# Performance work log

Hardware: AMD Instinct MI355X
Metric: run time of the kernel (lower is better)

The kernel has to match this reference:

```python
import jax, jax.numpy as jnp
import numpy as np

BN_EPS = 1e-5


def setup_inputs() -> dict:
    key = jax.random.key(0)
    ks = jax.random.split(key, 10)
    B, L, V, D = 4096, 200, 100000, 256
    tokens = jax.random.randint(ks[0], (B, L), 0, V, dtype=jnp.int32)
    lengths = jnp.maximum(jax.random.randint(ks[1], (B,), 0, L + 1, dtype=jnp.int32), 1)
    t = (jax.random.uniform(ks[2], (B,)) > 0.5).astype(jnp.float32)
    emb_table = jax.random.normal(ks[3], (V, D), dtype=jnp.float32)
    W1 = jax.random.normal(ks[4], (D, D), dtype=jnp.float32) * (1.0 / np.sqrt(D))
    b1 = jnp.zeros((D,), dtype=jnp.float32)
    gamma = jnp.ones((D,), dtype=jnp.float32)
    beta = jnp.zeros((D,), dtype=jnp.float32)
    w2 = jax.random.normal(ks[5], (D,), dtype=jnp.float32) * (1.0 / np.sqrt(D))
    b2 = jnp.zeros((), dtype=jnp.float32)
    return {"tokens": tokens, "lengths": lengths, "t": t, "emb_table": emb_table,
            "W1": W1, "b1": b1, "gamma": gamma, "beta": beta, "w2": w2, "b2": b2}


def reference(tokens, lengths, t, emb_table, W1, b1, gamma, beta, w2, b2):
    B, L = tokens.shape
    # ragged gather + mean pool (EmbeddingBag-mean equivalent)
    emb = emb_table[tokens]                                   # [B, L, D]
    mask = (jnp.arange(L)[None, :] < lengths[:, None]).astype(emb.dtype)  # [B, L]
    pooled = jnp.einsum('bld,bl->bd', emb, mask) / lengths[:, None].astype(emb.dtype)
    # fc_hidden -> BatchNorm1d (training-mode batch stats) -> ReLU (dropout = eval identity)
    z = pooled @ W1.T + b1                                    # [B, D]
    mu = jnp.mean(z, axis=0)
    var = jnp.var(z, axis=0)
    zn = (z - mu) / jnp.sqrt(var + BN_EPS)
    h = jax.nn.relu(gamma * zn + beta)
    # fc_output -> logits
    logits = h @ w2 + b2                                      # [B]
    # BCEWithLogitsLoss (mean, numerically stable)
    loss = jnp.mean(jnp.maximum(logits, 0.0) - logits * t + jnp.log1p(jnp.exp(-jnp.abs(logits))))
    return (loss, logits)
```

## Files before the change

kernel.cpp:

```cpp
#include <hip/hip_runtime.h>
#include <math.h>

#define L_ 200

__global__ __launch_bounds__(256) void pool_pack_kernel(
    const int* __restrict__ tokens, const int* __restrict__ lengths,
    const float* __restrict__ emb, float* __restrict__ pooled,
    const float* __restrict__ W1, float* __restrict__ W1p) {
  const int tid = threadIdx.x;
  if (blockIdx.x < 64) {
    float4 v = ((const float4*)W1)[tid * 64 + blockIdx.x];
    ((float4*)W1p)[blockIdx.x * 256 + tid] = v;
  }
  const int wv = tid >> 6, lane = tid & 63;
  const int row = blockIdx.x * 2 + (wv >> 1);
  const int half = wv & 1;
  const int len = lengths[row];
  const int* trow = tokens + row * L_;
  const float4* embv = (const float4*)emb;
  float4 a0 = make_float4(0.f, 0.f, 0.f, 0.f);
  float4 a1 = a0, a2 = a0, a3 = a0;
  for (int l0 = half * 64; l0 < len; l0 += 128) {
    int nt = len - l0; nt = nt > 64 ? 64 : nt;
    int tk = (lane < nt) ? trow[l0 + lane] : 0;
    int j = 0;
    for (; j + 4 <= nt; j += 4) {
      int t0 = __shfl(tk, j);
      int t1 = __shfl(tk, j + 1);
      int t2 = __shfl(tk, j + 2);
      int t3 = __shfl(tk, j + 3);
      float4 v0 = embv[(size_t)t0 * 64 + lane];
      float4 v1 = embv[(size_t)t1 * 64 + lane];
      float4 v2 = embv[(size_t)t2 * 64 + lane];
      float4 v3 = embv[(size_t)t3 * 64 + lane];
      a0.x += v0.x; a0.y += v0.y; a0.z += v0.z; a0.w += v0.w;
      a1.x += v1.x; a1.y += v1.y; a1.z += v1.z; a1.w += v1.w;
      a2.x += v2.x; a2.y += v2.y; a2.z += v2.z; a2.w += v2.w;
      a3.x += v3.x; a3.y += v3.y; a3.z += v3.z; a3.w += v3.w;
    }
    for (; j < nt; j++) {
      int t0 = __shfl(tk, j);
      float4 v0 = embv[(size_t)t0 * 64 + lane];
      a0.x += v0.x; a0.y += v0.y; a0.z += v0.z; a0.w += v0.w;
    }
  }
  float4 r;
  r.x = a0.x + a1.x + a2.x + a3.x;
  r.y = a0.y + a1.y + a2.y + a3.y;
  r.z = a0.z + a1.z + a2.z + a3.z;
  r.w = a0.w + a1.w + a2.w + a3.w;
  __shared__ float4 part[2][64];
  if (half) part[wv >> 1][lane] = r;
  __syncthreads();
  if (!half) {
    float4 o = part[wv >> 1][lane];
    const float inv = 1.0f / (float)len;
    r.x = (r.x + o.x) * inv;
    r.y = (r.y + o.y) * inv;
    r.z = (r.z + o.z) * inv;
    r.w = (r.w + o.w) * inv;
    ((float4*)pooled)[(size_t)row * 64 + lane] = r;
  }
}

__global__ __launch_bounds__(256) void gemm_stats_kernel(
    const float* __restrict__ pooled, const float* __restrict__ W1p,
    const float* __restrict__ b1, float* __restrict__ z,
    float* __restrict__ psum, float* __restrict__ psq) {
  __shared__ float4 SH[1024];
  const int tid = threadIdx.x;
  const int b0 = blockIdx.x * 16;
  const float4* pooled4 = (const float4*)pooled;
#pragma unroll
  for (int i = 0; i < 4; i++)
    SH[tid + i * 256] = pooled4[(size_t)b0 * 64 + tid + i * 256];
  __syncthreads();
  const int wv = tid >> 6, lane = tid & 63;
  const int r0 = wv * 4;
  float4 bb = ((const float4*)b1)[lane];
  float acc[4][4];
#pragma unroll
  for (int r = 0; r < 4; r++) {
    acc[r][0] = bb.x; acc[r][1] = bb.y; acc[r][2] = bb.z; acc[r][3] = bb.w;
  }
  const float4* w4 = (const float4*)W1p;
  for (int kb = 0; kb < 64; kb++) {
    float4 wk0 = w4[kb * 256 + lane * 4 + 0];
    float4 wk1 = w4[kb * 256 + lane * 4 + 1];
    float4 wk2 = w4[kb * 256 + lane * 4 + 2];
    float4 wk3 = w4[kb * 256 + lane * 4 + 3];
#pragma unroll
    for (int r = 0; r < 4; r++) {
      float4 p = SH[(r0 + r) * 64 + kb];
      acc[r][0] += p.x * wk0.x + p.y * wk0.y + p.z * wk0.z + p.w * wk0.w;
      acc[r][1] += p.x * wk1.x + p.y * wk1.y + p.z * wk1.z + p.w * wk1.w;
      acc[r][2] += p.x * wk2.x + p.y * wk2.y + p.z * wk2.z + p.w * wk2.w;
      acc[r][3] += p.x * wk3.x + p.y * wk3.y + p.z * wk3.z + p.w * wk3.w;
    }
  }
  float4* z4 = (float4*)z;
  float4 s = make_float4(0.f, 0.f, 0.f, 0.f), q = s;
#pragma unroll
  for (int r = 0; r < 4; r++) {
    float4 o = make_float4(acc[r][0], acc[r][1], acc[r][2], acc[r][3]);
    z4[(size_t)(b0 + r0 + r) * 64 + lane] = o;
    s.x += o.x; s.y += o.y; s.z += o.z; s.w += o.w;
    q.x += o.x * o.x; q.y += o.y * o.y; q.z += o.z * o.z; q.w += o.w * o.w;
  }
  __syncthreads();
  SH[wv * 64 + lane] = s;
  SH[256 + wv * 64 + lane] = q;
  __syncthreads();
  if (tid < 64) {
    float4 S = make_float4(0.f, 0.f, 0.f, 0.f), Q = S;
#pragma unroll
    for (int w = 0; w < 4; w++) {
      float4 a = SH[w * 64 + tid];
      float4 b = SH[256 + w * 64 + tid];
      S.x += a.x; S.y += a.y; S.z += a.z; S.w += a.w;
      Q.x += b.x; Q.y += b.y; Q.z += b.z; Q.w += b.w;
    }
    ((float4*)psum)[blockIdx.x * 64 + tid] = S;
    ((float4*)psq)[blockIdx.x * 64 + tid] = Q;
  }
}

__global__ __launch_bounds__(256) void bn_reduce_kernel(
    const float* __restrict__ psum, const float* __restrict__ psq,
    const float* __restrict__ gamma, const float* __restrict__ beta,
    float* __restrict__ A, float* __restrict__ C) {
  const int t = threadIdx.x;
  const int dd = t & 15, c = t >> 4;
  const int d = blockIdx.x * 16 + dd;
  float s = 0.f, q = 0.f;
#pragma unroll
  for (int i = 0; i < 16; i++) {
    int p = c * 16 + i;
    s += psum[p * 256 + d];
    q += psq[p * 256 + d];
  }
  __shared__ float sl[16][17], ql[16][17];
  sl[c][dd] = s; ql[c][dd] = q;
  __syncthreads();
  if (t < 16) {
    float S = 0.f, Q = 0.f;
#pragma unroll
    for (int c2 = 0; c2 < 16; c2++) { S += sl[c2][t]; Q += ql[c2][t]; }
    int dg = blockIdx.x * 16 + t;
    float m = S * (1.0f / 4096.0f);
    float v = Q * (1.0f / 4096.0f) - m * m;
    float a = gamma[dg] * rsqrtf(v + 1e-5f);
    A[dg] = a;
    C[dg] = beta[dg] - m * a;
  }
}

__global__ __launch_bounds__(256) void head_kernel(
    const float* __restrict__ z, const float* __restrict__ A,
    const float* __restrict__ C, const float* __restrict__ w2,
    const float* __restrict__ b2, const float* __restrict__ t,
    float* __restrict__ out, float* __restrict__ bce) {
  const int tid = threadIdx.x;
  const int wv = tid >> 6, lane = tid & 63;
  const int b = blockIdx.x * 4 + wv;
  float4 A4 = ((const float4*)A)[lane];
  float4 C4 = ((const float4*)C)[lane];
  float4 w24 = ((const float4*)w2)[lane];
  float4 zv = ((const float4*)z)[(size_t)b * 64 + lane];
  float h0 = fmaxf(A4.x * zv.x + C4.x, 0.f);
  float h1 = fmaxf(A4.y * zv.y + C4.y, 0.f);
  float h2 = fmaxf(A4.z * zv.z + C4.z, 0.f);
  float h3 = fmaxf(A4.w * zv.w + C4.w, 0.f);
  float part = h0 * w24.x + h1 * w24.y + h2 * w24.z + h3 * w24.w;
#pragma unroll
  for (int off = 32; off > 0; off >>= 1) part += __shfl_down(part, off);
  if (lane == 0) {
    float logit = part + b2[0];
    out[1 + b] = logit;
    float tb = t[b];
    bce[b] = fmaxf(logit, 0.f) - logit * tb + log1pf(expf(-fabsf(logit)));
  }
}

__global__ __launch_bounds__(256) void loss_kernel(const float* __restrict__ bce,
                                                   float* __restrict__ out) {
  __shared__ float red[4];
  const int tid = threadIdx.x;
  float s = 0.f;
  for (int i = 0; i < 16; i++) s += bce[tid + i * 256];
#pragma unroll
  for (int off = 32; off > 0; off >>= 1) s += __shfl_down(s, off);
  if ((tid & 63) == 0) red[tid >> 6] = s;
  __syncthreads();
  if (tid == 0) out[0] = (red[0] + red[1] + red[2] + red[3]) * (1.0f / 4096.0f);
}

extern "C" void kernel_launch(void* const* d_in, const int* in_sizes, int n_in,
                              void* d_out, int out_size, void* d_ws, size_t ws_size,
                              hipStream_t stream) {
  const int* tokens = (const int*)d_in[0];
  const int* lengths = (const int*)d_in[1];
  const float* t = (const float*)d_in[2];
  const float* emb = (const float*)d_in[3];
  const float* W1 = (const float*)d_in[4];
  const float* b1 = (const float*)d_in[5];
  const float* gamma = (const float*)d_in[6];
  const float* beta = (const float*)d_in[7];
  const float* w2 = (const float*)d_in[8];
  const float* b2 = (const float*)d_in[9];
  float* out = (float*)d_out;

  float* wsf = (float*)d_ws;
  float* pooled = wsf;
  float* z = wsf + 1048576;
  float* W1p = wsf + 2097152;
  float* psum = wsf + 2162688;
  float* psq = wsf + 2228224;
  float* A = wsf + 2293760;
  float* C = wsf + 2294016;
  float* bce = wsf + 2294272;

  pool_pack_kernel<<<2048, 256, 0, stream>>>(tokens, lengths, emb, pooled, W1, W1p);
  gemm_stats_kernel<<<256, 256, 0, stream>>>(pooled, W1p, b1, z, psum, psq);
  bn_reduce_kernel<<<16, 256, 0, stream>>>(psum, psq, gamma, beta, A, C);
  head_kernel<<<1024, 256, 0, stream>>>(z, A, C, w2, b2, t, out, bce);
  loss_kernel<<<1, 256, 0, stream>>>(bce, out);
}
```

Measured before the change: 239.0 us.

## Fuse all stages into one cooperative persistent kernel with grid syncs

Replaces the five separate launches with a single cooperative kernel of 256 blocks that loops over the pooling work, then runs GEMM+stats, BN reduction, the head and the loss, separated by grid.sync barriers. It also widens the gather unroll from 4 to 8 outstanding loads per iteration. The aim is to remove launch gaps and tail effects between the small kernels. The trade-off is that the memory-bound gather now runs on only 256 blocks (one per CU) instead of 2048, which may reduce latency hiding, and grid syncs add their own cost. If the cooperative launch fails, the code falls back to the old multi-kernel path.

Measured after the change: 396.3 us. 65.9% more time.

```diff
diff --git a/kernel.cpp b/kernel.cpp
--- a/kernel.cpp
+++ b/kernel.cpp
@@ -1,7 +1,229 @@
 #include <hip/hip_runtime.h>
+#include <hip/hip_cooperative_groups.h>
 #include <math.h>
 
+namespace cg = cooperative_groups;
+
 #define L_ 200
+
+__global__ __launch_bounds__(256) void fused_kernel(
+    const int* __restrict__ tokens, const int* __restrict__ lengths,
+    const float* __restrict__ t, const float* __restrict__ emb,
+    const float* __restrict__ W1, const float* __restrict__ b1,
+    const float* __restrict__ gamma, const float* __restrict__ beta,
+    const float* __restrict__ w2, const float* __restrict__ b2,
+    float* __restrict__ pooled, float* __restrict__ z, float* __restrict__ W1p,
+    float* __restrict__ psum, float* __restrict__ psq,
+    float* __restrict__ A, float* __restrict__ C,
+    float* __restrict__ bpart, float* __restrict__ out) {
+  cg::grid_group grid = cg::this_grid();
+  __shared__ float4 SH[1024];
+  float* SHf = (float*)SH;
+  const int tid = threadIdx.x;
+  const int wv = tid >> 6, lane = tid & 63;
+
+  const float4* embv = (const float4*)emb;
+  for (int vb = blockIdx.x; vb < 2048; vb += 256) {
+    if (vb < 64) {
+      float4 v = ((const float4*)W1)[tid * 64 + vb];
+      ((float4*)W1p)[vb * 256 + tid] = v;
+    }
+    const int row = vb * 2 + (wv >> 1);
+    const int half = wv & 1;
+    const int len = lengths[row];
+    const int* trow = tokens + row * L_;
+    float4 a0 = make_float4(0.f, 0.f, 0.f, 0.f);
+    float4 a1 = a0, a2 = a0, a3 = a0, a4 = a0, a5 = a0, a6 = a0, a7 = a0;
+    for (int l0 = half * 64; l0 < len; l0 += 128) {
+      int nt = len - l0; nt = nt > 64 ? 64 : nt;
+      int tk = (lane < nt) ? trow[l0 + lane] : 0;
+      int j = 0;
+      for (; j + 8 <= nt; j += 8) {
+        int t0 = __shfl(tk, j);
+        int t1 = __shfl(tk, j + 1);
+        int t2 = __shfl(tk, j + 2);
+        int t3 = __shfl(tk, j + 3);
+        int t4 = __shfl(tk, j + 4);
+        int t5 = __shfl(tk, j + 5);
+        int t6 = __shfl(tk, j + 6);
+        int t7 = __shfl(tk, j + 7);
+        float4 v0 = embv[(size_t)t0 * 64 + lane];
+        float4 v1 = embv[(size_t)t1 * 64 + lane];
+        float4 v2 = embv[(size_t)t2 * 64 + lane];
+        float4 v3 = embv[(size_t)t3 * 64 + lane];
+        float4 v4 = embv[(size_t)t4 * 64 + lane];
+        float4 v5 = embv[(size_t)t5 * 64 + lane];
+        float4 v6 = embv[(size_t)t6 * 64 + lane];
+        float4 v7 = embv[(size_t)t7 * 64 + lane];
+        a0.x += v0.x; a0.y += v0.y; a0.z += v0.z; a0.w += v0.w;
+        a1.x += v1.x; a1.y += v1.y; a1.z += v1.z; a1.w += v1.w;
+        a2.x += v2.x; a2.y += v2.y; a2.z += v2.z; a2.w += v2.w;
+        a3.x += v3.x; a3.y += v3.y; a3.z += v3.z; a3.w += v3.w;
+        a4.x += v4.x; a4.y += v4.y; a4.z += v4.z; a4.w += v4.w;
+        a5.x += v5.x; a5.y += v5.y; a5.z += v5.z; a5.w += v5.w;
+        a6.x += v6.x; a6.y += v6.y; a6.z += v6.z; a6.w += v6.w;
+        a7.x += v7.x; a7.y += v7.y; a7.z += v7.z; a7.w += v7.w;
+      }
+      for (; j + 4 <= nt; j += 4) {
+        int t0 = __shfl(tk, j);
+        int t1 = __shfl(tk, j + 1);
+        int t2 = __shfl(tk, j + 2);
+        int t3 = __shfl(tk, j + 3);
+        float4 v0 = embv[(size_t)t0 * 64 + lane];
+        float4 v1 = embv[(size_t)t1 * 64 + lane];
+        float4 v2 = embv[(size_t)t2 * 64 + lane];
+        float4 v3 = embv[(size_t)t3 * 64 + lane];
+        a0.x += v0.x; a0.y += v0.y; a0.z += v0.z; a0.w += v0.w;
+        a1.x += v1.x; a1.y += v1.y; a1.z += v1.z; a1.w += v1.w;
+        a2.x += v2.x; a2.y += v2.y; a2.z += v2.z; a2.w += v2.w;
+        a3.x += v3.x; a3.y += v3.y; a3.z += v3.z; a3.w += v3.w;
+      }
+      for (; j < nt; j++) {
+        int t0 = __shfl(tk, j);
+        float4 v0 = embv[(size_t)t0 * 64 + lane];
+        a0.x += v0.x; a0.y += v0.y; a0.z += v0.z; a0.w += v0.w;
+      }
+    }
+    float4 r;
+    r.x = ((a0.x + a1.x) + (a2.x + a3.x)) + ((a4.x + a5.x) + (a6.x + a7.x));
+    r.y = ((a0.y + a1.y) + (a2.y + a3.y)) + ((a4.y + a5.y) + (a6.y + a7.y));
+    r.z = ((a0.z + a1.z) + (a2.z + a3.z)) + ((a4.z + a5.z) + (a6.z + a7.z));
+    r.w = ((a0.w + a1.w) + (a2.w + a3.w)) + ((a4.w + a5.w) + (a6.w + a7.w));
+    __syncthreads();
+    if (half) SH[(wv >> 1) * 64 + lane] = r;
+    __syncthreads();
+    if (!half) {
+      float4 o = SH[(wv >> 1) * 64 + lane];
+      const float inv = 1.0f / (float)len;
+      r.x = (r.x + o.x) * inv;
+      r.y = (r.y + o.y) * inv;
+      r.z = (r.z + o.z) * inv;
+      r.w = (r.w + o.w) * inv;
+      ((float4*)pooled)[(size_t)row * 64 + lane] = r;
+    }
+  }
+  grid.sync();
+
+  {
+    const int b0 = blockIdx.x * 16;
+    const float4* pooled4 = (const float4*)pooled;
+#pragma unroll
+    for (int i = 0; i < 4; i++)
+      SH[tid + i * 256] = pooled4[(size_t)b0 * 64 + tid + i * 256];
+    __syncthreads();
+    const int r0 = wv * 4;
+    float4 bb = ((const float4*)b1)[lane];
+    float acc[4][4];
+#pragma unroll
+    for (int r = 0; r < 4; r++) {
+      acc[r][0] = bb.x; acc[r][1] = bb.y; acc[r][2] = bb.z; acc[r][3] = bb.w;
+    }
+    const float4* w4 = (const float4*)W1p;
+    for (int kb = 0; kb < 64; kb++) {
+      float4 wk0 = w4[kb * 256 + lane * 4 + 0];
+      float4 wk1 = w4[kb * 256 + lane * 4 + 1];
+      float4 wk2 = w4[kb * 256 + lane * 4 + 2];
+      float4 wk3 = w4[kb * 256 + lane * 4 + 3];
+#pragma unroll
+      for (int r = 0; r < 4; r++) {
+        float4 p = SH[(r0 + r) * 64 + kb];
+        acc[r][0] += p.x * wk0.x + p.y * wk0.y + p.z * wk0.z + p.w * wk0.w;
+        acc[r][1] += p.x * wk1.x + p.y * wk1.y + p.z * wk1.z + p.w * wk1.w;
+        acc[r][2] += p.x * wk2.x + p.y * wk2.y + p.z * wk2.z + p.w * wk2.w;
+        acc[r][3] += p.x * wk3.x + p.y * wk3.y + p.z * wk3.z + p.w * wk3.w;
+      }
+    }
+    float4* z4 = (float4*)z;
+    float4 s = make_float4(0.f, 0.f, 0.f, 0.f), q = s;
+#pragma unroll
+    for (int r = 0; r < 4; r++) {
+      float4 o = make_float4(acc[r][0], acc[r][1], acc[r][2], acc[r][3]);
+      z4[(size_t)(b0 + r0 + r) * 64 + lane] = o;
+      s.x += o.x; s.y += o.y; s.z += o.z; s.w += o.w;
+      q.x += o.x * o.x; q.y += o.y * o.y; q.z += o.z * o.z; q.w += o.w * o.w;
+    }
+    __syncthreads();
+    SH[wv * 64 + lane] = s;
+    SH[256 + wv * 64 + lane] = q;
+    __syncthreads();
+    if (tid < 64) {
+      float4 S = make_float4(0.f, 0.f, 0.f, 0.f), Q = S;
+#pragma unroll
+      for (int w = 0; w < 4; w++) {
+        float4 a = SH[w * 64 + tid];
+        float4 b = SH[256 + w * 64 + tid];
+        S.x += a.x; S.y += a.y; S.z += a.z; S.w += a.w;
+        Q.x += b.x; Q.y += b.y; Q.z += b.z; Q.w += b.w;
+      }
+      ((float4*)psum)[blockIdx.x * 64 + tid] = S;
+      ((float4*)psq)[blockIdx.x * 64 + tid] = Q;
+    }
+  }
+  grid.sync();
+
+  {
+    const int d = blockIdx.x;
+    float s = psum[tid * 256 + d];
+    float q = psq[tid * 256 + d];
+#pragma unroll
+    for (int off = 32; off > 0; off >>= 1) {
+      s += __shfl_down(s, off);
+      q += __shfl_down(q, off);
+    }
+    if (lane == 0) { SHf[wv] = s; SHf[8 + wv] = q; }
+    __syncthreads();
+    if (tid == 0) {
+      float S = (SHf[0] + SHf[1]) + (SHf[2] + SHf[3]);
+      float Q = (SHf[8] + SHf[9]) + (SHf[10] + SHf[11]);
+      float m = S * (1.0f / 4096.0f);
+      float v = Q * (1.0f / 4096.0f) - m * m;
+      float a = gamma[d] * rsqrtf(v + 1e-5f);
+      A[d] = a;
+      C[d] = beta[d] - m * a;
+    }
+  }
+  grid.sync();
+
+  {
+    float4 A4 = ((const float4*)A)[lane];
+    float4 C4 = ((const float4*)C)[lane];
+    float4 w24 = ((const float4*)w2)[lane];
+    float b2v = b2[0];
+    float bsum = 0.f;
+    for (int hb = blockIdx.x; hb < 1024; hb += 256) {
+      const int b = hb * 4 + wv;
+      float4 zv = ((const float4*)z)[(size_t)b * 64 + lane];
+      float h0 = fmaxf(A4.x * zv.x + C4.x, 0.f);
+      float h1 = fmaxf(A4.y * zv.y + C4.y, 0.f);
+      float h2 = fmaxf(A4.z * zv.z + C4.z, 0.f);
+      float h3 = fmaxf(A4.w * zv.w + C4.w, 0.f);
+      float part = h0 * w24.x + h1 * w24.y + h2 * w24.z + h3 * w24.w;
+#pragma unroll
+      for (int off = 32; off > 0; off >>= 1) part += __shfl_down(part, off);
+      if (lane == 0) {
+        float logit = part + b2v;
+        out[1 + b] = logit;
+        float tb = t[b];
+        bsum += fmaxf(logit, 0.f) - logit * tb + log1pf(expf(-fabsf(logit)));
+      }
+    }
+    __syncthreads();
+    if (lane == 0) SHf[wv] = bsum;
+    __syncthreads();
+    if (tid == 0) bpart[blockIdx.x] = (SHf[0] + SHf[1]) + (SHf[2] + SHf[3]);
+  }
+  grid.sync();
+
+  if (blockIdx.x == 0) {
+    float s = bpart[tid];
+#pragma unroll
+    for (int off = 32; off > 0; off >>= 1) s += __shfl_down(s, off);
+    __syncthreads();
+    if (lane == 0) SHf[wv] = s;
+    __syncthreads();
+    if (tid == 0) out[0] = ((SHf[0] + SHf[1]) + (SHf[2] + SHf[3])) * (1.0f / 4096.0f);
+  }
+}
 
 __global__ __launch_bounds__(256) void pool_pack_kernel(
     const int* __restrict__ tokens, const int* __restrict__ lengths,
@@ -219,10 +441,21 @@
   float* A = wsf + 2293760;
   float* C = wsf + 2294016;
   float* bce = wsf + 2294272;
-
-  pool_pack_kernel<<<2048, 256, 0, stream>>>(tokens, lengths, emb, pooled, W1, W1p);
-  gemm_stats_kernel<<<256, 256, 0, stream>>>(pooled, W1p, b1, z, psum, psq);
-  bn_reduce_kernel<<<16, 256, 0, stream>>>(psum, psq, gamma, beta, A, C);
-  head_kernel<<<1024, 256, 0, stream>>>(z, A, C, w2, b2, t, out, bce);
-  loss_kernel<<<1, 256, 0, stream>>>(bce, out);
-}
+  float* bpart = wsf + 2298368;
+
+  void* args[] = {(void*)&tokens, (void*)&lengths, (void*)&t, (void*)&emb,
+                  (void*)&W1, (void*)&b1, (void*)&gamma, (void*)&beta,
+                  (void*)&w2, (void*)&b2, (void*)&pooled, (void*)&z,
+                  (void*)&W1p, (void*)&psum, (void*)&psq, (void*)&A,
+                  (void*)&C, (void*)&bpart, (void*)&out};
+  hipError_t err = hipLaunchCooperativeKernel((void*)fused_kernel, dim3(256),
+                                              dim3(256), args, 0, stream);
+  if (err != hipSuccess) {
+    (void)hipGetLastError();
+    pool_pack_kernel<<<2048, 256, 0, stream>>>(tokens, lengths, emb, pooled, W1, W1p);
+    gemm_stats_kernel<<<256, 256, 0, stream>>>(pooled, W1p, b1, z, psum, psq);
+    bn_reduce_kernel<<<16, 256, 0, stream>>>(psum, psq, gamma, beta, A, C);
+    head_kernel<<<1024, 256, 0, stream>>>(z, A, C, w2, b2, t, out, bce);
+    loss_kernel<<<1, 256, 0, stream>>>(bce, out);
+  }
+}
```

## Fuse embedding pooling with the W1 GEMM and BN partial stats per block

Applied to the files above, without the earlier changes.

The pooling kernel now computes the two pooled rows in shared memory and immediately multiplies them by W1, with the K dimension split across the four waves and reduced in LDS. This removes the pooled intermediate round-trip and the separate GEMM launch, and writes transposed per-block BN partials so the reduce kernel reads them contiguously. W1 packing moves to its own small kernel. The trade-off is that each of the 2048 blocks rereads the full 256 KB W1 (served mostly from L2), and there are now 2048 partials per feature instead of 256.

New measurement: 242.7 us. No clear change (+1.6%).

```diff
diff --git a/kernel.cpp b/kernel.cpp
--- a/kernel.cpp
+++ b/kernel.cpp
@@ -3,21 +3,29 @@
 
 #define L_ 200
 
-__global__ __launch_bounds__(256) void pool_pack_kernel(
+__global__ __launch_bounds__(256) void pack_kernel(const float* __restrict__ W1,
+                                                   float* __restrict__ W1p) {
+  const int tid = threadIdx.x;
+  float4 v = ((const float4*)W1)[tid * 64 + blockIdx.x];
+  ((float4*)W1p)[blockIdx.x * 256 + tid] = v;
+}
+
+__global__ __launch_bounds__(256) void pool_gemm_kernel(
     const int* __restrict__ tokens, const int* __restrict__ lengths,
-    const float* __restrict__ emb, float* __restrict__ pooled,
-    const float* __restrict__ W1, float* __restrict__ W1p) {
-  const int tid = threadIdx.x;
-  if (blockIdx.x < 64) {
-    float4 v = ((const float4*)W1)[tid * 64 + blockIdx.x];
-    ((float4*)W1p)[blockIdx.x * 256 + tid] = v;
-  }
+    const float* __restrict__ emb, const float* __restrict__ W1p,
+    const float* __restrict__ b1, float* __restrict__ z,
+    float* __restrict__ psumT, float* __restrict__ psqT) {
+  __shared__ float4 PART[2][64];
+  __shared__ float4 SHP[2][64];
+  __shared__ float4 SRED4[4][2][64];
+  const int tid = threadIdx.x;
   const int wv = tid >> 6, lane = tid & 63;
-  const int row = blockIdx.x * 2 + (wv >> 1);
-  const int half = wv & 1;
+  const int pair = wv >> 1, half = wv & 1;
+  const int row = blockIdx.x * 2 + pair;
   const int len = lengths[row];
   const int* trow = tokens + row * L_;
   const float4* embv = (const float4*)emb;
+
   float4 a0 = make_float4(0.f, 0.f, 0.f, 0.f);
   float4 a1 = a0, a2 = a0, a3 = a0;
   for (int l0 = half * 64; l0 < len; l0 += 128) {
@@ -45,113 +53,93 @@
     }
   }
   float4 r;
-  r.x = a0.x + a1.x + a2.x + a3.x;
-  r.y = a0.y + a1.y + a2.y + a3.y;
-  r.z = a0.z + a1.z + a2.z + a3.z;
-  r.w = a0.w + a1.w + a2.w + a3.w;
-  __shared__ float4 part[2][64];
-  if (half) part[wv >> 1][lane] = r;
+  r.x = (a0.x + a1.x) + (a2.x + a3.x);
+  r.y = (a0.y + a1.y) + (a2.y + a3.y);
+  r.z = (a0.z + a1.z) + (a2.z + a3.z);
+  r.w = (a0.w + a1.w) + (a2.w + a3.w);
+  if (half) PART[pair][lane] = r;
   __syncthreads();
   if (!half) {
-    float4 o = part[wv >> 1][lane];
+    float4 o = PART[pair][lane];
     const float inv = 1.0f / (float)len;
     r.x = (r.x + o.x) * inv;
     r.y = (r.y + o.y) * inv;
     r.z = (r.z + o.z) * inv;
     r.w = (r.w + o.w) * inv;
-    ((float4*)pooled)[(size_t)row * 64 + lane] = r;
-  }
-}
-
-__global__ __launch_bounds__(256) void gemm_stats_kernel(
-    const float* __restrict__ pooled, const float* __restrict__ W1p,
-    const float* __restrict__ b1, float* __restrict__ z,
-    float* __restrict__ psum, float* __restrict__ psq) {
-  __shared__ float4 SH[1024];
-  const int tid = threadIdx.x;
-  const int b0 = blockIdx.x * 16;
-  const float4* pooled4 = (const float4*)pooled;
-#pragma unroll
-  for (int i = 0; i < 4; i++)
-    SH[tid + i * 256] = pooled4[(size_t)b0 * 64 + tid + i * 256];
-  __syncthreads();
-  const int wv = tid >> 6, lane = tid & 63;
-  const int r0 = wv * 4;
-  float4 bb = ((const float4*)b1)[lane];
-  float acc[4][4];
-#pragma unroll
-  for (int r = 0; r < 4; r++) {
-    acc[r][0] = bb.x; acc[r][1] = bb.y; acc[r][2] = bb.z; acc[r][3] = bb.w;
-  }
+    SHP[pair][lane] = r;
+  }
+  __syncthreads();
+
   const float4* w4 = (const float4*)W1p;
-  for (int kb = 0; kb < 64; kb++) {
+  float acc0[4] = {0.f, 0.f, 0.f, 0.f};
+  float acc1[4] = {0.f, 0.f, 0.f, 0.f};
+  const int kb0 = wv * 16;
+  for (int kk = 0; kk < 16; kk++) {
+    const int kb = kb0 + kk;
+    float4 p0 = SHP[0][kb];
+    float4 p1 = SHP[1][kb];
     float4 wk0 = w4[kb * 256 + lane * 4 + 0];
     float4 wk1 = w4[kb * 256 + lane * 4 + 1];
     float4 wk2 = w4[kb * 256 + lane * 4 + 2];
     float4 wk3 = w4[kb * 256 + lane * 4 + 3];
-#pragma unroll
-    for (int r = 0; r < 4; r++) {
-      float4 p = SH[(r0 + r) * 64 + kb];
-      acc[r][0] += p.x * wk0.x + p.y * wk0.y + p.z * wk0.z + p.w * wk0.w;
-      acc[r][1] += p.x * wk1.x + p.y * wk1.y + p.z * wk1.z + p.w * wk1.w;
-      acc[r][2] += p.x * wk2.x + p.y * wk2.y + p.z * wk2.z + p.w * wk2.w;
-      acc[r][3] += p.x * wk3.x + p.y * wk3.y + p.z * wk3.z + p.w * wk3.w;
-    }
-  }
-  float4* z4 = (float4*)z;
-  float4 s = make_float4(0.f, 0.f, 0.f, 0.f), q = s;
-#pragma unroll
-  for (int r = 0; r < 4; r++) {
-    float4 o = make_float4(acc[r][0], acc[r][1], acc[r][2], acc[r][3]);
-    z4[(size_t)(b0 + r0 + r) * 64 + lane] = o;
-    s.x += o.x; s.y += o.y; s.z += o.z; s.w += o.w;
-    q.x += o.x * o.x; q.y += o.y * o.y; q.z += o.z * o.z; q.w += o.w * o.w;
-  }
-  __syncthreads();
-  SH[wv * 64 + lane] = s;
-  SH[256 + wv * 64 + lane] = q;
-  __syncthreads();
-  if (tid < 64) {
-    float4 S = make_float4(0.f, 0.f, 0.f, 0.f), Q = S;
-#pragma unroll
-    for (int w = 0; w < 4; w++) {
-      float4 a = SH[w * 64 + tid];
-      float4 b = SH[256 + w * 64 + tid];
-      S.x += a.x; S.y += a.y; S.z += a.z; S.w += a.w;
-      Q.x += b.x; Q.y += b.y; Q.z += b.z; Q.w += b.w;
-    }
-    ((float4*)psum)[blockIdx.x * 64 + tid] = S;
-    ((float4*)psq)[blockIdx.x * 64 + tid] = Q;
-  }
+    acc0[0] += p0.x * wk0.x + p0.y * wk0.y + p0.z * wk0.z + p0.w * wk0.w;
+    acc0[1] += p0.x * wk1.x + p0.y * wk1.y + p0.z * wk1.z + p0.w * wk1.w;
+    acc0[2] += p0.x * wk2.x + p0.y * wk2.y + p0.z * wk2.z + p0.w * wk2.w;
+    acc0[3] += p0.x * wk3.x + p0.y * wk3.y + p0.z * wk3.z + p0.w * wk3.w;
+    acc1[0] += p1.x * wk0.x + p1.y * wk0.y + p1.z * wk0.z + p1.w * wk0.w;
+    acc1[1] += p1.x * wk1.x + p1.y * wk1.y + p1.z * wk1.z + p1.w * wk1.w;
+    acc1[2] += p1.x * wk2.x + p1.y * wk2.y + p1.z * wk2.z + p1.w * wk2.w;
+    acc1[3] += p1.x * wk3.x + p1.y * wk3.y + p1.z * wk3.z + p1.w * wk3.w;
+  }
+  SRED4[wv][0][lane] = make_float4(acc0[0], acc0[1], acc0[2], acc0[3]);
+  SRED4[wv][1][lane] = make_float4(acc1[0], acc1[1], acc1[2], acc1[3]);
+  __syncthreads();
+  const float* SREDf = (const float*)SRED4;
+  const float bb = b1[tid];
+  float z0 = bb, z1 = bb;
+#pragma unroll
+  for (int w = 0; w < 4; w++) {
+    z0 += SREDf[(w * 2 + 0) * 256 + tid];
+    z1 += SREDf[(w * 2 + 1) * 256 + tid];
+  }
+  const int r0 = blockIdx.x * 2;
+  z[(size_t)r0 * 256 + tid] = z0;
+  z[(size_t)(r0 + 1) * 256 + tid] = z1;
+  psumT[(size_t)tid * 2048 + blockIdx.x] = z0 + z1;
+  psqT[(size_t)tid * 2048 + blockIdx.x] = z0 * z0 + z1 * z1;
 }
 
 __global__ __launch_bounds__(256) void bn_reduce_kernel(
-    const float* __restrict__ psum, const float* __restrict__ psq,
+    const float* __restrict__ psumT, const float* __restrict__ psqT,
     const float* __restrict__ gamma, const float* __restrict__ beta,
     float* __restrict__ A, float* __restrict__ C) {
-  const int t = threadIdx.x;
-  const int dd = t & 15, c = t >> 4;
-  const int d = blockIdx.x * 16 + dd;
+  const int tid = threadIdx.x;
+  const int wv = tid >> 6, lane = tid & 63;
+  const int d = blockIdx.x;
+  const float* ps = psumT + (size_t)d * 2048;
+  const float* pq = psqT + (size_t)d * 2048;
   float s = 0.f, q = 0.f;
 #pragma unroll
-  for (int i = 0; i < 16; i++) {
-    int p = c * 16 + i;
-    s += psum[p * 256 + d];
-    q += psq[p * 256 + d];
-  }
-  __shared__ float sl[16][17], ql[16][17];
-  sl[c][dd] = s; ql[c][dd] = q;
-  __syncthreads();
-  if (t < 16) {
-    float S = 0.f, Q = 0.f;
-#pragma unroll
-    for (int c2 = 0; c2 < 16; c2++) { S += sl[c2][t]; Q += ql[c2][t]; }
-    int dg = blockIdx.x * 16 + t;
+  for (int i = 0; i < 8; i++) {
+    s += ps[i * 256 + tid];
+    q += pq[i * 256 + tid];
+  }
+#pragma unroll
+  for (int off = 32; off > 0; off >>= 1) {
+    s += __shfl_down(s, off);
+    q += __shfl_down(q, off);
+  }
+  __shared__ float sl[4], ql[4];
+  if (lane == 0) { sl[wv] = s; ql[wv] = q; }
+  __syncthreads();
+  if (tid == 0) {
+    float S = (sl[0] + sl[1]) + (sl[2] + sl[3]);
+    float Q = (ql[0] + ql[1]) + (ql[2] + ql[3]);
     float m = S * (1.0f / 4096.0f);
     float v = Q * (1.0f / 4096.0f) - m * m;
-    float a = gamma[dg] * rsqrtf(v + 1e-5f);
-    A[dg] = a;
-    C[dg] = beta[dg] - m * a;
+    float a = gamma[d] * rsqrtf(v + 1e-5f);
+    A[d] = a;
+    C[d] = beta[d] - m * a;
   }
 }
 
@@ -211,18 +199,18 @@
   float* out = (float*)d_out;
 
   float* wsf = (float*)d_ws;
-  float* pooled = wsf;
-  float* z = wsf + 1048576;
-  float* W1p = wsf + 2097152;
-  float* psum = wsf + 2162688;
-  float* psq = wsf + 2228224;
-  float* A = wsf + 2293760;
-  float* C = wsf + 2294016;
-  float* bce = wsf + 2294272;
-
-  pool_pack_kernel<<<2048, 256, 0, stream>>>(tokens, lengths, emb, pooled, W1, W1p);
-  gemm_stats_kernel<<<256, 256, 0, stream>>>(pooled, W1p, b1, z, psum, psq);
-  bn_reduce_kernel<<<16, 256, 0, stream>>>(psum, psq, gamma, beta, A, C);
+  float* z = wsf;
+  float* W1p = wsf + 1048576;
+  float* psumT = wsf + 1114112;
+  float* psqT = wsf + 1638400;
+  float* A = wsf + 2162688;
+  float* C = wsf + 2162944;
+  float* bce = wsf + 2163200;
+
+  pack_kernel<<<64, 256, 0, stream>>>(W1, W1p);
+  pool_gemm_kernel<<<2048, 256, 0, stream>>>(tokens, lengths, emb, W1p, b1,
+                                             z, psumT, psqT);
+  bn_reduce_kernel<<<256, 256, 0, stream>>>(psumT, psqT, gamma, beta, A, C);
   head_kernel<<<1024, 256, 0, stream>>>(z, A, C, w2, b2, t, out, bce);
   loss_kernel<<<1, 256, 0, stream>>>(bce, out);
 }
```

## Fuse BN reduce and loss into preceding kernels via last-block atomics

Applied to the files above, without the earlier changes.

Removes two small kernel launches by folding the BatchNorm statistic reduction into the GEMM kernel and the BCE loss reduction into the head kernel. Each uses an atomic counter so the last finishing block does the final reduction, with counters zeroed in the pool kernel. The pool kernel also interleaves tokens between its two wavefronts (even and odd positions) so the work splits evenly for short rows. The cost is a serial 256-iteration reduction done by a single block, plus the threadfence and atomic overhead.

After: 340.7 us. 42.6% more time.

```diff
diff --git a/kernel.cpp b/kernel.cpp
--- a/kernel.cpp
+++ b/kernel.cpp
@@ -6,8 +6,10 @@
 __global__ __launch_bounds__(256) void pool_pack_kernel(
     const int* __restrict__ tokens, const int* __restrict__ lengths,
     const float* __restrict__ emb, float* __restrict__ pooled,
-    const float* __restrict__ W1, float* __restrict__ W1p) {
+    const float* __restrict__ W1, float* __restrict__ W1p,
+    int* __restrict__ cnts) {
   const int tid = threadIdx.x;
+  if (blockIdx.x == 0 && tid < 8) cnts[tid] = 0;
   if (blockIdx.x < 64) {
     float4 v = ((const float4*)W1)[tid * 64 + blockIdx.x];
     ((float4*)W1p)[blockIdx.x * 256 + tid] = v;
@@ -16,13 +18,14 @@
   const int row = blockIdx.x * 2 + (wv >> 1);
   const int half = wv & 1;
   const int len = lengths[row];
+  const int cnt = (len + 1 - half) >> 1;
   const int* trow = tokens + row * L_;
   const float4* embv = (const float4*)emb;
   float4 a0 = make_float4(0.f, 0.f, 0.f, 0.f);
   float4 a1 = a0, a2 = a0, a3 = a0;
-  for (int l0 = half * 64; l0 < len; l0 += 128) {
-    int nt = len - l0; nt = nt > 64 ? 64 : nt;
-    int tk = (lane < nt) ? trow[l0 + lane] : 0;
+  for (int b0 = 0; b0 < cnt; b0 += 64) {
+    int nt = cnt - b0; nt = nt > 64 ? 64 : nt;
+    int tk = (lane < nt) ? trow[half + 2 * (b0 + lane)] : 0;
     int j = 0;
     for (; j + 4 <= nt; j += 4) {
       int t0 = __shfl(tk, j);
@@ -45,10 +48,10 @@
     }
   }
   float4 r;
-  r.x = a0.x + a1.x + a2.x + a3.x;
-  r.y = a0.y + a1.y + a2.y + a3.y;
-  r.z = a0.z + a1.z + a2.z + a3.z;
-  r.w = a0.w + a1.w + a2.w + a3.w;
+  r.x = (a0.x + a1.x) + (a2.x + a3.x);
+  r.y = (a0.y + a1.y) + (a2.y + a3.y);
+  r.z = (a0.z + a1.z) + (a2.z + a3.z);
+  r.w = (a0.w + a1.w) + (a2.w + a3.w);
   __shared__ float4 part[2][64];
   if (half) part[wv >> 1][lane] = r;
   __syncthreads();
@@ -63,10 +66,12 @@
   }
 }
 
-__global__ __launch_bounds__(256) void gemm_stats_kernel(
+__global__ __launch_bounds__(256) void gemm_stats_bn_kernel(
     const float* __restrict__ pooled, const float* __restrict__ W1p,
     const float* __restrict__ b1, float* __restrict__ z,
-    float* __restrict__ psum, float* __restrict__ psq) {
+    float* __restrict__ psum, float* __restrict__ psq,
+    const float* __restrict__ gamma, const float* __restrict__ beta,
+    float* __restrict__ A, float* __restrict__ C, int* __restrict__ cnts) {
   __shared__ float4 SH[1024];
   const int tid = threadIdx.x;
   const int b0 = blockIdx.x * 16;
@@ -123,43 +128,30 @@
     ((float4*)psum)[blockIdx.x * 64 + tid] = S;
     ((float4*)psq)[blockIdx.x * 64 + tid] = Q;
   }
-}
-
-__global__ __launch_bounds__(256) void bn_reduce_kernel(
-    const float* __restrict__ psum, const float* __restrict__ psq,
-    const float* __restrict__ gamma, const float* __restrict__ beta,
-    float* __restrict__ A, float* __restrict__ C) {
-  const int t = threadIdx.x;
-  const int dd = t & 15, c = t >> 4;
-  const int d = blockIdx.x * 16 + dd;
-  float s = 0.f, q = 0.f;
-#pragma unroll
-  for (int i = 0; i < 16; i++) {
-    int p = c * 16 + i;
-    s += psum[p * 256 + d];
-    q += psq[p * 256 + d];
-  }
-  __shared__ float sl[16][17], ql[16][17];
-  sl[c][dd] = s; ql[c][dd] = q;
-  __syncthreads();
-  if (t < 16) {
+  __shared__ int isLast;
+  __threadfence();
+  if (tid == 0) isLast = (atomicAdd(&cnts[0], 1) == 255);
+  __syncthreads();
+  if (isLast) {
+    __threadfence();
     float S = 0.f, Q = 0.f;
-#pragma unroll
-    for (int c2 = 0; c2 < 16; c2++) { S += sl[c2][t]; Q += ql[c2][t]; }
-    int dg = blockIdx.x * 16 + t;
+    for (int b = 0; b < 256; b++) {
+      S += psum[b * 256 + tid];
+      Q += psq[b * 256 + tid];
+    }
     float m = S * (1.0f / 4096.0f);
     float v = Q * (1.0f / 4096.0f) - m * m;
-    float a = gamma[dg] * rsqrtf(v + 1e-5f);
-    A[dg] = a;
-    C[dg] = beta[dg] - m * a;
-  }
-}
-
-__global__ __launch_bounds__(256) void head_kernel(
+    float a = gamma[tid] * rsqrtf(v + 1e-5f);
+    A[tid] = a;
+    C[tid] = beta[tid] - m * a;
+  }
+}
+
+__global__ __launch_bounds__(256) void head_loss_kernel(
     const float* __restrict__ z, const float* __restrict__ A,
     const float* __restrict__ C, const float* __restrict__ w2,
     const float* __restrict__ b2, const float* __restrict__ t,
-    float* __restrict__ out, float* __restrict__ bce) {
+    float* __restrict__ out, float* __restrict__ bpart, int* __restrict__ cnts) {
   const int tid = threadIdx.x;
   const int wv = tid >> 6, lane = tid & 63;
   const int b = blockIdx.x * 4 + wv;
@@ -174,25 +166,33 @@
   float part = h0 * w24.x + h1 * w24.y + h2 * w24.z + h3 * w24.w;
 #pragma unroll
   for (int off = 32; off > 0; off >>= 1) part += __shfl_down(part, off);
+  __shared__ float red[4];
   if (lane == 0) {
     float logit = part + b2[0];
     out[1 + b] = logit;
     float tb = t[b];
-    bce[b] = fmaxf(logit, 0.f) - logit * tb + log1pf(expf(-fabsf(logit)));
-  }
-}
-
-__global__ __launch_bounds__(256) void loss_kernel(const float* __restrict__ bce,
-                                                   float* __restrict__ out) {
-  __shared__ float red[4];
-  const int tid = threadIdx.x;
-  float s = 0.f;
-  for (int i = 0; i < 16; i++) s += bce[tid + i * 256];
-#pragma unroll
-  for (int off = 32; off > 0; off >>= 1) s += __shfl_down(s, off);
-  if ((tid & 63) == 0) red[tid >> 6] = s;
-  __syncthreads();
-  if (tid == 0) out[0] = (red[0] + red[1] + red[2] + red[3]) * (1.0f / 4096.0f);
+    red[wv] = fmaxf(logit, 0.f) - logit * tb + log1pf(expf(-fabsf(logit)));
+  }
+  __syncthreads();
+  if (tid == 0)
+    bpart[blockIdx.x] = (red[0] + red[1]) + (red[2] + red[3]);
+  __shared__ int isLast;
+  __threadfence();
+  if (tid == 0) isLast = (atomicAdd(&cnts[1], 1) == 1023);
+  __syncthreads();
+  if (isLast) {
+    __threadfence();
+    float s = 0.f;
+#pragma unroll
+    for (int i = 0; i < 4; i++) s += bpart[tid + i * 256];
+#pragma unroll
+    for (int off = 32; off > 0; off >>= 1) s += __shfl_down(s, off);
+    __shared__ float fin[4];
+    if (lane == 0) fin[wv] = s;
+    __syncthreads();
+    if (tid == 0)
+      out[0] = ((fin[0] + fin[1]) + (fin[2] + fin[3])) * (1.0f / 4096.0f);
+  }
 }
 
 extern "C" void kernel_launch(void* const* d_in, const int* in_sizes, int n_in,
@@ -218,11 +218,12 @@
   float* psq = wsf + 2228224;
   float* A = wsf + 2293760;
   float* C = wsf + 2294016;
-  float* bce = wsf + 2294272;
-
-  pool_pack_kernel<<<2048, 256, 0, stream>>>(tokens, lengths, emb, pooled, W1, W1p);
-  gemm_stats_kernel<<<256, 256, 0, stream>>>(pooled, W1p, b1, z, psum, psq);
-  bn_reduce_kernel<<<16, 256, 0, stream>>>(psum, psq, gamma, beta, A, C);
-  head_kernel<<<1024, 256, 0, stream>>>(z, A, C, w2, b2, t, out, bce);
-  loss_kernel<<<1, 256, 0, stream>>>(bce, out);
-}
+  float* bpart = wsf + 2294272;
+  int* cnts = (int*)(wsf + 2295296);
+
+  pool_pack_kernel<<<2048, 256, 0, stream>>>(tokens, lengths, emb, pooled,
+                                             W1, W1p, cnts);
+  gemm_stats_bn_kernel<<<256, 256, 0, stream>>>(pooled, W1p, b1, z, psum, psq,
+                                                gamma, beta, A, C, cnts);
+  head_loss_kernel<<<1024, 256, 0, stream>>>(z, A, C, w2, b2, t, out, bpart, cnts);
+}
```
